# Optimization experiments

Measured on AMD Instinct MI355X. Metric: run time of the kernel, lower is better.

Reference implementation:

```python
import jax, jax.numpy as jnp
import numpy as np

HIDDEN = 2048
N_HEADS = 32
N_KV_HEADS = 4
HEAD_DIM = 128
EPS = 1e-6
ROPE_THETA = 1000000.0
B, S = 1, 2048


def setup_inputs() -> dict:
    key = jax.random.key(0)
    ks = jax.random.split(key, 7)
    scale = 0.02
    return {
        "hidden_states": jax.random.normal(ks[0], (B, S, HIDDEN), jnp.float32),
        "wq": jax.random.normal(ks[1], (HIDDEN, N_HEADS * HEAD_DIM), jnp.float32) * scale,
        "wk": jax.random.normal(ks[2], (HIDDEN, N_KV_HEADS * HEAD_DIM), jnp.float32) * scale,
        "wv": jax.random.normal(ks[3], (HIDDEN, N_KV_HEADS * HEAD_DIM), jnp.float32) * scale,
        "wo": jax.random.normal(ks[4], (N_HEADS * HEAD_DIM, HIDDEN), jnp.float32) * scale,
        "q_norm_w": jnp.ones((HEAD_DIM,), jnp.float32),
        "k_norm_w": jnp.ones((HEAD_DIM,), jnp.float32),
    }


def _rmsnorm(x, w, eps=EPS):
    # RMSNorm over last (head_dim) axis, as in Qwen3MoeRMSNorm applied per-head
    var = jnp.mean(jnp.square(x), axis=-1, keepdims=True)
    return x * jax.lax.rsqrt(var + eps) * w


def _rope_cos_sin(seq_len, dtype):
    inv_freq = 1.0 / (ROPE_THETA ** (jnp.arange(0, HEAD_DIM, 2, dtype=jnp.float32) / HEAD_DIM))
    pos = jnp.arange(seq_len, dtype=jnp.float32)
    freqs = pos[:, None] * inv_freq[None, :]          # [S, dh/2]
    emb = jnp.concatenate([freqs, freqs], axis=-1)    # [S, dh]
    return jnp.cos(emb).astype(dtype), jnp.sin(emb).astype(dtype)


def _rotate_half(x):
    h = x.shape[-1] // 2
    return jnp.concatenate([-x[..., h:], x[..., :h]], axis=-1)


def reference(hidden_states, wq, wk, wv, wo, q_norm_w, k_norm_w):
    b, s, _ = hidden_states.shape
    # QKV projections (bias-free)
    q = (hidden_states @ wq).reshape(b, s, N_HEADS, HEAD_DIM)
    k = (hidden_states @ wk).reshape(b, s, N_KV_HEADS, HEAD_DIM)
    v = (hidden_states @ wv).reshape(b, s, N_KV_HEADS, HEAD_DIM)
    # per-head RMSNorm on Q and K
    q = _rmsnorm(q, q_norm_w)
    k = _rmsnorm(k, k_norm_w)
    # RoPE (prefill, start_pos = 0)
    cos, sin = _rope_cos_sin(s, q.dtype)              # [S, dh]
    cos = cos[None, :, None, :]
    sin = sin[None, :, None, :]
    q = q * cos + _rotate_half(q) * sin
    k = k * cos + _rotate_half(k) * sin
    # GQA: repeat KV heads to match Q heads
    groups = N_HEADS // N_KV_HEADS
    k = jnp.repeat(k, groups, axis=2)                 # [B,S,nH,dh]
    v = jnp.repeat(v, groups, axis=2)
    # causal SDPA
    scaling = HEAD_DIM ** -0.5
    scores = jnp.einsum("bqhd,bkhd->bhqk", q, k) * scaling
    causal = jnp.tril(jnp.ones((s, s), dtype=bool))
    scores = jnp.where(causal[None, None], scores, jnp.finfo(scores.dtype).min)
    probs = jax.nn.softmax(scores, axis=-1)
    attn = jnp.einsum("bhqk,bkhd->bqhd", probs, v)    # [B,S,nH,dh]
    attn = attn.reshape(b, s, N_HEADS * HEAD_DIM)
    return attn @ wo
```

## Files before the change

kernel.cpp:

```cpp
#include <hip/hip_runtime.h>
#include <stdint.h>

typedef unsigned short u16;
typedef __bf16 bf16x8 __attribute__((ext_vector_type(8)));
typedef float f32x4 __attribute__((ext_vector_type(4)));

#define SEQ 2048
#define QKV_N 5120
#define QN 4096

#if __has_builtin(__builtin_amdgcn_exp2f)
#define EXP2F __builtin_amdgcn_exp2f
#else
#define EXP2F exp2f
#endif

#define QSC (0.08838834764831845f * 1.4426950408889634f)
#define MLOG2E 17.312340490667560f

__device__ __forceinline__ u16 f2bf(float f) {
  union { float f; unsigned u; } v; v.f = f;
  unsigned r = v.u + 0x7fffu + ((v.u >> 16) & 1u);
  return (u16)(r >> 16);
}
__device__ __forceinline__ u16 f2bf_fast(float f) {
  union { float f; unsigned u; } v; v.f = f;
  return (u16)((v.u + 0x8000u) >> 16);
}

__device__ __forceinline__ void gl2lds16(const void* g, void* l) {
  __builtin_amdgcn_global_load_lds((const __attribute__((address_space(1))) void*)g,
                                   (__attribute__((address_space(3))) void*)l, 16, 0, 0);
}

__global__ __launch_bounds__(256) void k_convert(const float* __restrict__ src, u16* __restrict__ dst) {
  int i = (blockIdx.x * 256 + threadIdx.x) * 4;
  float4 v = *(const float4*)(src + i);
  ushort4 o;
  o.x = f2bf(v.x); o.y = f2bf(v.y); o.z = f2bf(v.z); o.w = f2bf(v.w);
  *(ushort4*)(dst + i) = o;
}

__global__ __launch_bounds__(256) void k_transpose(const float* __restrict__ src, u16* __restrict__ dst,
                                                   int R, int C) {
  __shared__ float t[32][33];
  int c0 = blockIdx.x * 32, r0 = blockIdx.y * 32;
  int j = threadIdx.x & 31, i0 = threadIdx.x >> 5;
#pragma unroll
  for (int p = 0; p < 4; ++p) {
    int r = i0 + p * 8;
    t[r][j] = src[(size_t)(r0 + r) * C + c0 + j];
  }
  __syncthreads();
#pragma unroll
  for (int p = 0; p < 4; ++p) {
    int r = i0 + p * 8;
    dst[(size_t)(c0 + r) * R + r0 + j] = f2bf(t[j][r]);
  }
}

__global__ __launch_bounds__(256) void k_gemm_bt(const u16* __restrict__ A, const u16* __restrict__ BT,
                                                 float* __restrict__ C, int M, int N, int K) {
  __shared__ u16 As[128 * 64];
  __shared__ u16 Bs[128 * 64];
  const int tid = threadIdx.x;
  const int w = tid >> 6, lane = tid & 63, quad = lane >> 4, l15 = lane & 15;
  const int m0 = blockIdx.y * 128, n0 = blockIdx.x * 128;
  const int mw = (w & 1) * 64, nw = (w >> 1) * 64;

  f32x4 acc[4][4];
#pragma unroll
  for (int i = 0; i < 4; ++i)
#pragma unroll
    for (int j = 0; j < 4; ++j) acc[i][j] = {0.f, 0.f, 0.f, 0.f};

  const int nk = K >> 6;
  for (int kt = 0; kt < nk; ++kt) {
    const int k0 = kt << 6;
    __syncthreads();
#pragma unroll
    for (int p = 0; p < 4; ++p) {
      int ci = (w * 4 + p) * 64 + lane;
      int row = ci >> 3, pc = ci & 7, gc = pc ^ (row & 7);
      gl2lds16(A + (size_t)(m0 + row) * K + k0 + gc * 8, As + (w * 4 + p) * 512);
      gl2lds16(BT + (size_t)(n0 + row) * K + k0 + gc * 8, Bs + (w * 4 + p) * 512);
    }
    __syncthreads();
#pragma unroll
    for (int kk = 0; kk < 2; ++kk) {
      bf16x8 a[4], b[4];
#pragma unroll
      for (int mt = 0; mt < 4; ++mt) {
        int row = mw + mt * 16 + l15;
        int col = ((kk * 4 + quad) ^ (row & 7)) * 8;
        a[mt] = *(const bf16x8*)(As + row * 64 + col);
      }
#pragma unroll
      for (int nt = 0; nt < 4; ++nt) {
        int row = nw + nt * 16 + l15;
        int col = ((kk * 4 + quad) ^ (row & 7)) * 8;
        b[nt] = *(const bf16x8*)(Bs + row * 64 + col);
      }
#pragma unroll
      for (int mt = 0; mt < 4; ++mt)
#pragma unroll
        for (int nt = 0; nt < 4; ++nt)
          acc[mt][nt] = __builtin_amdgcn_mfma_f32_16x16x32_bf16(a[mt], b[nt], acc[mt][nt], 0, 0, 0);
    }
  }
#pragma unroll
  for (int mt = 0; mt < 4; ++mt)
#pragma unroll
    for (int nt = 0; nt < 4; ++nt)
#pragma unroll
      for (int r = 0; r < 4; ++r) {
        int row = m0 + mw + mt * 16 + quad * 4 + r;
        int col = n0 + nw + nt * 16 + l15;
        C[(size_t)row * N + col] = acc[mt][nt][r];
      }
}

__global__ __launch_bounds__(256) void k_gemm_bt64(const u16* __restrict__ A, const u16* __restrict__ BT,
                                                   float* __restrict__ C, int M, int N, int K) {
  __shared__ u16 As[64 * 64];
  __shared__ u16 Bs[128 * 64];
  const int tid = threadIdx.x;
  const int w = tid >> 6, lane = tid & 63, quad = lane >> 4, l15 = lane & 15;
  const int m0 = blockIdx.y * 64, n0 = blockIdx.x * 128;
  const int nw = w * 32;

  f32x4 acc[4][2];
#pragma unroll
  for (int i = 0; i < 4; ++i)
#pragma unroll
    for (int j = 0; j < 2; ++j) acc[i][j] = {0.f, 0.f, 0.f, 0.f};

  const int nk = K >> 6;
  for (int kt = 0; kt < nk; ++kt) {
    const int k0 = kt << 6;
    __syncthreads();
#pragma unroll
    for (int p = 0; p < 2; ++p) {
      int ci = p * 256 + tid;
      int row = ci >> 3, gc = (ci & 7) ^ (row & 7);
      gl2lds16(A + (size_t)(m0 + row) * K + k0 + gc * 8, As + (p * 256 + w * 64) * 8);
    }
#pragma unroll
    for (int p = 0; p < 4; ++p) {
      int ci = p * 256 + tid;
      int row = ci >> 3, gc = (ci & 7) ^ (row & 7);
      gl2lds16(BT + (size_t)(n0 + row) * K + k0 + gc * 8, Bs + (p * 256 + w * 64) * 8);
    }
    __syncthreads();
#pragma unroll
    for (int kk = 0; kk < 2; ++kk) {
      bf16x8 a[4], b[2];
#pragma unroll
      for (int mt = 0; mt < 4; ++mt) {
        int row = mt * 16 + l15;
        a[mt] = *(const bf16x8*)(As + row * 64 + (((kk * 4 + quad) ^ (row & 7)) * 8));
      }
#pragma unroll
      for (int nt = 0; nt < 2; ++nt) {
        int row = nw + nt * 16 + l15;
        b[nt] = *(const bf16x8*)(Bs + row * 64 + (((kk * 4 + quad) ^ (row & 7)) * 8));
      }
#pragma unroll
      for (int mt = 0; mt < 4; ++mt)
#pragma unroll
        for (int nt = 0; nt < 2; ++nt)
          acc[mt][nt] = __builtin_amdgcn_mfma_f32_16x16x32_bf16(a[mt], b[nt], acc[mt][nt], 0, 0, 0);
    }
  }
#pragma unroll
  for (int mt = 0; mt < 4; ++mt)
#pragma unroll
    for (int nt = 0; nt < 2; ++nt)
#pragma unroll
      for (int r = 0; r < 4; ++r) {
        int row = m0 + mt * 16 + quad * 4 + r;
        int col = n0 + nw + nt * 16 + l15;
        C[(size_t)row * N + col] = acc[mt][nt][r];
      }
}

__global__ __launch_bounds__(256) void k_postproc(const float* __restrict__ QKV,
                                                  const float* __restrict__ qw, const float* __restrict__ kw,
                                                  u16* __restrict__ qb, u16* __restrict__ kb) {
  int s = blockIdx.x;
  int w = threadIdx.x >> 6, lane = threadIdx.x & 63;
  const float* row = QKV + (size_t)s * QKV_N;
  float inv_freq = EXP2F(-(float)lane * (19.931568569324174f / 64.0f));
  float fr = (float)s * inv_freq;
  float sn, cs;
  __sincosf(fr, &sn, &cs);
  float qw0 = qw[lane], qw1 = qw[lane + 64];
  float kw0 = kw[lane], kw1 = kw[lane + 64];
  for (int item = w; item < 36; item += 4) {
    bool isq = item < 32;
    int h = isq ? item : item - 32;
    int base = isq ? h * 128 : 4096 + h * 128;
    float x0 = row[base + lane], x1 = row[base + 64 + lane];
    float ss = x0 * x0 + x1 * x1;
#pragma unroll
    for (int off = 1; off < 64; off <<= 1) ss += __shfl_xor(ss, off);
    float rr = rsqrtf(ss * (1.0f / 128.0f) + 1e-6f);
    float n0 = x0 * rr * (isq ? qw0 : kw0), n1 = x1 * rr * (isq ? qw1 : kw1);
    float y0 = n0 * cs - n1 * sn;
    float y1 = n1 * cs + n0 * sn;
    if (isq) {
      size_t o = (size_t)s * QN + h * 128 + lane;
      qb[o] = f2bf(y0 * QSC);
      qb[o + 64] = f2bf(y1 * QSC);
    } else {
      size_t o = ((size_t)h * SEQ + s) * 128 + lane;
      kb[o] = f2bf(y0);
      kb[o + 64] = f2bf(y1);
    }
  }
}

__global__ __launch_bounds__(256) void k_vtrans(const float* __restrict__ QKV, u16* __restrict__ vt) {
  __shared__ float t[32][33];
  int s0 = blockIdx.x * 32, d0 = blockIdx.y * 32, h = blockIdx.z;
  int j = threadIdx.x & 31, i0 = threadIdx.x >> 5;
#pragma unroll
  for (int p = 0; p < 4; ++p) {
    int r = i0 + p * 8;
    t[r][j] = QKV[(size_t)(s0 + r) * QKV_N + 4608 + h * 128 + d0 + j];
  }
  __syncthreads();
#pragma unroll
  for (int p = 0; p < 4; ++p) {
    int r = i0 + p * 8;
    vt[((size_t)h * 128 + d0 + r) * SEQ + s0 + j] = f2bf(t[j][r]);
  }
}

__global__ __launch_bounds__(256, 2) void k_flash(const u16* __restrict__ qb_, const u16* __restrict__ kb,
                                                  const u16* __restrict__ vt, u16* __restrict__ attn) {
  __shared__ u16 Ks[64 * 128];
  __shared__ u16 Vts[128 * 64];
  __shared__ u16 Ps[4][2048];
  const int bx = blockIdx.x;
  const int slot = bx & 255, phase = bx >> 8;
  const int head = slot & 31;
  const int qblk = phase ? (slot >> 5) : 15 - (slot >> 5);
  const int kvh = head >> 3;
  const int q0 = qblk * 128;
  const int tid = threadIdx.x, w = tid >> 6, lane = tid & 63, quad = lane >> 4, l15 = lane & 15;
  const int rowlo0 = q0 + w * 32, rowlo1 = rowlo0 + 16;

  bf16x8 qf[2][4];
#pragma unroll
  for (int mt = 0; mt < 2; ++mt) {
    const u16* qrow = qb_ + (size_t)(rowlo0 + mt * 16 + l15) * QN + head * 128;
#pragma unroll
    for (int ks = 0; ks < 4; ++ks) qf[mt][ks] = *(const bf16x8*)(qrow + ks * 32 + quad * 8);
  }
  f32x4 o[2][8];
#pragma unroll
  for (int mt = 0; mt < 2; ++mt)
#pragma unroll
    for (int i = 0; i < 8; ++i) o[mt][i] = {0.f, 0.f, 0.f, 0.f};
  float lr[2][4] = {{0.f, 0.f, 0.f, 0.f}, {0.f, 0.f, 0.f, 0.f}};

  const u16* kbase = kb + (size_t)kvh * SEQ * 128;
  const u16* vbase = vt + (size_t)kvh * 128 * SEQ;
  u16* pw = Ps[w];

  const int nT = 2 * qblk + 2;
  for (int ti = 0; ti < nT; ++ti) {
    const int t0 = ti * 64;
    __syncthreads();
#pragma unroll
    for (int p = 0; p < 4; ++p) {
      int ci = (w * 4 + p) * 64 + lane;
      {
        int row = ci >> 4, pc = ci & 15, gc = pc ^ (row & 15);
        gl2lds16(kbase + (size_t)(t0 + row) * 128 + gc * 8, Ks + (w * 4 + p) * 512);
      }
      {
        int d = ci >> 3, pc = ci & 7, gc = pc ^ (d & 7);
        gl2lds16(vbase + (size_t)d * SEQ + t0 + gc * 8, Vts + (w * 4 + p) * 512);
      }
    }
    __syncthreads();

    const bool a0 = t0 < rowlo0 + 16;
    const bool a1 = t0 < rowlo1 + 16;
    if (a1) {
      f32x4 sa[2][4];
#pragma unroll
      for (int mt = 0; mt < 2; ++mt)
#pragma unroll
        for (int nt = 0; nt < 4; ++nt) sa[mt][nt] = {0.f, 0.f, 0.f, 0.f};
#pragma unroll
      for (int nt = 0; nt < 4; ++nt) {
        int row = nt * 16 + l15;
#pragma unroll
        for (int ks = 0; ks < 4; ++ks) {
          bf16x8 kf = *(const bf16x8*)(Ks + row * 128 + (((ks * 4 + quad) ^ (row & 15)) * 8));
          if (a0) sa[0][nt] = __builtin_amdgcn_mfma_f32_16x16x32_bf16(qf[0][ks], kf, sa[0][nt], 0, 0, 0);
          sa[1][nt] = __builtin_amdgcn_mfma_f32_16x16x32_bf16(qf[1][ks], kf, sa[1][nt], 0, 0, 0);
        }
      }
#pragma unroll
      for (int mt = 0; mt < 2; ++mt) {
        if (mt == 0 && !a0) continue;
        const int rl = rowlo0 + mt * 16;
        const bool domask = (t0 + 63 > rl);
        u16* pm = pw + mt * 1024;
#pragma unroll
        for (int nt = 0; nt < 4; ++nt)
#pragma unroll
          for (int r = 0; r < 4; ++r) {
            float p = EXP2F(sa[mt][nt][r] - MLOG2E);
            if (domask) {
              int tcol = t0 + nt * 16 + l15;
              int qrow = rl + quad * 4 + r;
              p = (tcol > qrow) ? 0.f : p;
            }
            sa[mt][nt][r] = p;
            pm[(quad * 4 + r) * 64 + ((nt ^ quad) << 4) + l15] = f2bf_fast(p);
          }
#pragma unroll
        for (int r = 0; r < 4; ++r)
          lr[mt][r] += sa[mt][0][r] + sa[mt][1][r] + sa[mt][2][r] + sa[mt][3][r];
      }
      asm volatile("s_waitcnt lgkmcnt(0)" ::: "memory");
#pragma unroll
      for (int ks2 = 0; ks2 < 2; ++ks2) {
        int col = (ks2 * 32 + quad * 8) ^ ((l15 >> 2) << 4);
        bf16x8 pa0, pa1;
        if (a0) pa0 = *(const bf16x8*)(pw + l15 * 64 + col);
        pa1 = *(const bf16x8*)(pw + 1024 + l15 * 64 + col);
#pragma unroll
        for (int nt2 = 0; nt2 < 8; ++nt2) {
          int d = nt2 * 16 + l15;
          bf16x8 vf = *(const bf16x8*)(Vts + d * 64 + (((ks2 * 4 + quad) ^ (d & 7)) * 8));
          if (a0) o[0][nt2] = __builtin_amdgcn_mfma_f32_16x16x32_bf16(pa0, vf, o[0][nt2], 0, 0, 0);
          o[1][nt2] = __builtin_amdgcn_mfma_f32_16x16x32_bf16(pa1, vf, o[1][nt2], 0, 0, 0);
        }
      }
    }
  }
#pragma unroll
  for (int mt = 0; mt < 2; ++mt) {
    float inv[4];
#pragma unroll
    for (int r = 0; r < 4; ++r) {
      float s = lr[mt][r];
      s += __shfl_xor(s, 1);
      s += __shfl_xor(s, 2);
      s += __shfl_xor(s, 4);
      s += __shfl_xor(s, 8);
      inv[r] = 1.0f / s;
    }
#pragma unroll
    for (int nt2 = 0; nt2 < 8; ++nt2)
#pragma unroll
      for (int r = 0; r < 4; ++r) {
        size_t idx = (size_t)(rowlo0 + mt * 16 + quad * 4 + r) * QN + head * 128 + nt2 * 16 + l15;
        attn[idx] = f2bf_fast(o[mt][nt2][r] * inv[r]);
      }
  }
}

extern "C" void kernel_launch(void* const* d_in, const int* in_sizes, int n_in,
                              void* d_out, int out_size, void* d_ws, size_t ws_size,
                              hipStream_t stream) {
  const float* hidden = (const float*)d_in[0];
  const float* wq = (const float*)d_in[1];
  const float* wk = (const float*)d_in[2];
  const float* wv = (const float*)d_in[3];
  const float* wo = (const float*)d_in[4];
  const float* qnw = (const float*)d_in[5];
  const float* knw = (const float*)d_in[6];
  float* out = (float*)d_out;

  char* ws = (char*)d_ws;
  u16* hid_bf = (u16*)(ws);
  u16* WT = (u16*)(ws + 8388608);
  u16* woT = (u16*)(ws + 29360128);
  float* QKV = (float*)(ws + 46137344);
  u16* q_bf = (u16*)(ws + 88080384);
  u16* k_bf = (u16*)(ws + 104857600);
  u16* vt = (u16*)(ws + 106954752);
  u16* attn = (u16*)(ws + 109051904);

  k_convert<<<4096, 256, 0, stream>>>(hidden, hid_bf);
  k_transpose<<<dim3(128, 64), 256, 0, stream>>>(wq, WT, 2048, 4096);
  k_transpose<<<dim3(16, 64), 256, 0, stream>>>(wk, WT + (size_t)4096 * 2048, 2048, 512);
  k_transpose<<<dim3(16, 64), 256, 0, stream>>>(wv, WT + (size_t)4608 * 2048, 2048, 512);
  k_transpose<<<dim3(64, 128), 256, 0, stream>>>(wo, woT, 4096, 2048);
  k_gemm_bt<<<dim3(40, 16), 256, 0, stream>>>(hid_bf, WT, QKV, 2048, 5120, 2048);
  k_postproc<<<2048, 256, 0, stream>>>(QKV, qnw, knw, q_bf, k_bf);
  k_vtrans<<<dim3(64, 4, 4), 256, 0, stream>>>(QKV, vt);
  k_flash<<<512, 256, 0, stream>>>(q_bf, k_bf, vt, attn);
  k_gemm_bt64<<<dim3(16, 32), 256, 0, stream>>>(attn, woT, out, 2048, 2048, 4096);
}
```

Measured before the change: 362.1 us.

## Retile QKV GEMM to 160-wide tiles with bf16 output and split-K output projection

The QKV projection now uses 128x160 tiles, giving a 32x16 grid of 512 blocks instead of 640, and stores bf16 rather than fp32. This halves the QKV intermediate traffic read by the postprocess and V-transpose kernels. The output projection switches from 64-row tiles to 128x128 tiles with split-K over two halves, accumulating with atomicAdd into an output zeroed by a memset. In exchange it adds an extra memset, atomic write traffic, and bf16 rounding of the QKV values before RMSNorm.

Result: faster. 340.9 us (-5.9%).

```diff
diff --git a/kernel.cpp b/kernel.cpp
--- a/kernel.cpp
+++ b/kernel.cpp
@@ -26,6 +26,10 @@
 __device__ __forceinline__ u16 f2bf_fast(float f) {
   union { float f; unsigned u; } v; v.f = f;
   return (u16)((v.u + 0x8000u) >> 16);
+}
+__device__ __forceinline__ float bf2f(u16 b) {
+  union { unsigned u; float f; } v; v.u = ((unsigned)b) << 16;
+  return v.f;
 }
 
 __device__ __forceinline__ void gl2lds16(const void* g, void* l) {
@@ -59,7 +63,71 @@
   }
 }
 
-__global__ __launch_bounds__(256) void k_gemm_bt(const u16* __restrict__ A, const u16* __restrict__ BT,
+__global__ __launch_bounds__(256) void k_gemm160(const u16* __restrict__ A, const u16* __restrict__ BT,
+                                                 u16* __restrict__ C, int M, int N, int K) {
+  __shared__ u16 As[128 * 64];
+  __shared__ u16 Bs[160 * 64];
+  const int tid = threadIdx.x;
+  const int w = tid >> 6, lane = tid & 63, quad = lane >> 4, l15 = lane & 15;
+  const int m0 = blockIdx.y * 128, n0 = blockIdx.x * 160;
+  const int mw = (w & 1) * 64, nw = (w >> 1) * 80;
+
+  f32x4 acc[4][5];
+#pragma unroll
+  for (int i = 0; i < 4; ++i)
+#pragma unroll
+    for (int j = 0; j < 5; ++j) acc[i][j] = {0.f, 0.f, 0.f, 0.f};
+
+  const int nk = K >> 6;
+  for (int kt = 0; kt < nk; ++kt) {
+    const int k0 = kt << 6;
+    __syncthreads();
+#pragma unroll
+    for (int p = 0; p < 4; ++p) {
+      int ci = (w * 4 + p) * 64 + lane;
+      int row = ci >> 3, gc = (ci & 7) ^ (row & 7);
+      gl2lds16(A + (size_t)(m0 + row) * K + k0 + gc * 8, As + (w * 4 + p) * 512);
+    }
+#pragma unroll
+    for (int p = 0; p < 5; ++p) {
+      int ci = (w * 5 + p) * 64 + lane;
+      int row = ci >> 3, gc = (ci & 7) ^ (row & 7);
+      gl2lds16(BT + (size_t)(n0 + row) * K + k0 + gc * 8, Bs + (w * 5 + p) * 512);
+    }
+    __syncthreads();
+#pragma unroll
+    for (int kk = 0; kk < 2; ++kk) {
+      bf16x8 a[4], b[5];
+#pragma unroll
+      for (int mt = 0; mt < 4; ++mt) {
+        int row = mw + mt * 16 + l15;
+        a[mt] = *(const bf16x8*)(As + row * 64 + (((kk * 4 + quad) ^ (row & 7)) * 8));
+      }
+#pragma unroll
+      for (int nt = 0; nt < 5; ++nt) {
+        int row = nw + nt * 16 + l15;
+        b[nt] = *(const bf16x8*)(Bs + row * 64 + (((kk * 4 + quad) ^ (row & 7)) * 8));
+      }
+#pragma unroll
+      for (int mt = 0; mt < 4; ++mt)
+#pragma unroll
+        for (int nt = 0; nt < 5; ++nt)
+          acc[mt][nt] = __builtin_amdgcn_mfma_f32_16x16x32_bf16(a[mt], b[nt], acc[mt][nt], 0, 0, 0);
+    }
+  }
+#pragma unroll
+  for (int mt = 0; mt < 4; ++mt)
+#pragma unroll
+    for (int nt = 0; nt < 5; ++nt)
+#pragma unroll
+      for (int r = 0; r < 4; ++r) {
+        int row = m0 + mw + mt * 16 + quad * 4 + r;
+        int col = n0 + nw + nt * 16 + l15;
+        C[(size_t)row * N + col] = f2bf(acc[mt][nt][r]);
+      }
+}
+
+__global__ __launch_bounds__(256) void k_gemm_sk(const u16* __restrict__ A, const u16* __restrict__ BT,
                                                  float* __restrict__ C, int M, int N, int K) {
   __shared__ u16 As[128 * 64];
   __shared__ u16 Bs[128 * 64];
@@ -67,6 +135,8 @@
   const int w = tid >> 6, lane = tid & 63, quad = lane >> 4, l15 = lane & 15;
   const int m0 = blockIdx.y * 128, n0 = blockIdx.x * 128;
   const int mw = (w & 1) * 64, nw = (w >> 1) * 64;
+  const int khalf = K >> 1;
+  const int kbase = blockIdx.z * khalf;
 
   f32x4 acc[4][4];
 #pragma unroll
@@ -74,14 +144,14 @@
 #pragma unroll
     for (int j = 0; j < 4; ++j) acc[i][j] = {0.f, 0.f, 0.f, 0.f};
 
-  const int nk = K >> 6;
+  const int nk = khalf >> 6;
   for (int kt = 0; kt < nk; ++kt) {
-    const int k0 = kt << 6;
+    const int k0 = kbase + (kt << 6);
     __syncthreads();
 #pragma unroll
     for (int p = 0; p < 4; ++p) {
       int ci = (w * 4 + p) * 64 + lane;
-      int row = ci >> 3, pc = ci & 7, gc = pc ^ (row & 7);
+      int row = ci >> 3, gc = (ci & 7) ^ (row & 7);
       gl2lds16(A + (size_t)(m0 + row) * K + k0 + gc * 8, As + (w * 4 + p) * 512);
       gl2lds16(BT + (size_t)(n0 + row) * K + k0 + gc * 8, Bs + (w * 4 + p) * 512);
     }
@@ -92,14 +162,12 @@
 #pragma unroll
       for (int mt = 0; mt < 4; ++mt) {
         int row = mw + mt * 16 + l15;
-        int col = ((kk * 4 + quad) ^ (row & 7)) * 8;
-        a[mt] = *(const bf16x8*)(As + row * 64 + col);
+        a[mt] = *(const bf16x8*)(As + row * 64 + (((kk * 4 + quad) ^ (row & 7)) * 8));
       }
 #pragma unroll
       for (int nt = 0; nt < 4; ++nt) {
         int row = nw + nt * 16 + l15;
-        int col = ((kk * 4 + quad) ^ (row & 7)) * 8;
-        b[nt] = *(const bf16x8*)(Bs + row * 64 + col);
+        b[nt] = *(const bf16x8*)(Bs + row * 64 + (((kk * 4 + quad) ^ (row & 7)) * 8));
       }
 #pragma unroll
       for (int mt = 0; mt < 4; ++mt)
@@ -116,80 +184,16 @@
       for (int r = 0; r < 4; ++r) {
         int row = m0 + mw + mt * 16 + quad * 4 + r;
         int col = n0 + nw + nt * 16 + l15;
-        C[(size_t)row * N + col] = acc[mt][nt][r];
-      }
-}
-
-__global__ __launch_bounds__(256) void k_gemm_bt64(const u16* __restrict__ A, const u16* __restrict__ BT,
-                                                   float* __restrict__ C, int M, int N, int K) {
-  __shared__ u16 As[64 * 64];
-  __shared__ u16 Bs[128 * 64];
-  const int tid = threadIdx.x;
-  const int w = tid >> 6, lane = tid & 63, quad = lane >> 4, l15 = lane & 15;
-  const int m0 = blockIdx.y * 64, n0 = blockIdx.x * 128;
-  const int nw = w * 32;
-
-  f32x4 acc[4][2];
-#pragma unroll
-  for (int i = 0; i < 4; ++i)
-#pragma unroll
-    for (int j = 0; j < 2; ++j) acc[i][j] = {0.f, 0.f, 0.f, 0.f};
-
-  const int nk = K >> 6;
-  for (int kt = 0; kt < nk; ++kt) {
-    const int k0 = kt << 6;
-    __syncthreads();
-#pragma unroll
-    for (int p = 0; p < 2; ++p) {
-      int ci = p * 256 + tid;
-      int row = ci >> 3, gc = (ci & 7) ^ (row & 7);
-      gl2lds16(A + (size_t)(m0 + row) * K + k0 + gc * 8, As + (p * 256 + w * 64) * 8);
-    }
-#pragma unroll
-    for (int p = 0; p < 4; ++p) {
-      int ci = p * 256 + tid;
-      int row = ci >> 3, gc = (ci & 7) ^ (row & 7);
-      gl2lds16(BT + (size_t)(n0 + row) * K + k0 + gc * 8, Bs + (p * 256 + w * 64) * 8);
-    }
-    __syncthreads();
-#pragma unroll
-    for (int kk = 0; kk < 2; ++kk) {
-      bf16x8 a[4], b[2];
-#pragma unroll
-      for (int mt = 0; mt < 4; ++mt) {
-        int row = mt * 16 + l15;
-        a[mt] = *(const bf16x8*)(As + row * 64 + (((kk * 4 + quad) ^ (row & 7)) * 8));
-      }
-#pragma unroll
-      for (int nt = 0; nt < 2; ++nt) {
-        int row = nw + nt * 16 + l15;
-        b[nt] = *(const bf16x8*)(Bs + row * 64 + (((kk * 4 + quad) ^ (row & 7)) * 8));
-      }
-#pragma unroll
-      for (int mt = 0; mt < 4; ++mt)
-#pragma unroll
-        for (int nt = 0; nt < 2; ++nt)
-          acc[mt][nt] = __builtin_amdgcn_mfma_f32_16x16x32_bf16(a[mt], b[nt], acc[mt][nt], 0, 0, 0);
-    }
-  }
-#pragma unroll
-  for (int mt = 0; mt < 4; ++mt)
-#pragma unroll
-    for (int nt = 0; nt < 2; ++nt)
-#pragma unroll
-      for (int r = 0; r < 4; ++r) {
-        int row = m0 + mt * 16 + quad * 4 + r;
-        int col = n0 + nw + nt * 16 + l15;
-        C[(size_t)row * N + col] = acc[mt][nt][r];
-      }
-}
-
-__global__ __launch_bounds__(256) void k_postproc(const float* __restrict__ QKV,
+        atomicAdd(&C[(size_t)row * N + col], acc[mt][nt][r]);
+      }
+}
+
+__global__ __launch_bounds__(256) void k_postproc(const u16* __restrict__ QKV,
                                                   const float* __restrict__ qw, const float* __restrict__ kw,
                                                   u16* __restrict__ qb, u16* __restrict__ kb) {
   int s = blockIdx.x;
   int w = threadIdx.x >> 6, lane = threadIdx.x & 63;
-  const float* row = QKV + (size_t)s * QKV_N;
+  const u16* row = QKV + (size_t)s * QKV_N;
   float inv_freq = EXP2F(-(float)lane * (19.931568569324174f / 64.0f));
   float fr = (float)s * inv_freq;
   float sn, cs;
@@ -200,7 +204,7 @@
     bool isq = item < 32;
     int h = isq ? item : item - 32;
     int base = isq ? h * 128 : 4096 + h * 128;
-    float x0 = row[base + lane], x1 = row[base + 64 + lane];
+    float x0 = bf2f(row[base + lane]), x1 = bf2f(row[base + 64 + lane]);
     float ss = x0 * x0 + x1 * x1;
 #pragma unroll
     for (int off = 1; off < 64; off <<= 1) ss += __shfl_xor(ss, off);
@@ -220,8 +224,8 @@
   }
 }
 
-__global__ __launch_bounds__(256) void k_vtrans(const float* __restrict__ QKV, u16* __restrict__ vt) {
-  __shared__ float t[32][33];
+__global__ __launch_bounds__(256) void k_vtrans(const u16* __restrict__ QKV, u16* __restrict__ vt) {
+  __shared__ u16 t[32][34];
   int s0 = blockIdx.x * 32, d0 = blockIdx.y * 32, h = blockIdx.z;
   int j = threadIdx.x & 31, i0 = threadIdx.x >> 5;
 #pragma unroll
@@ -233,7 +237,7 @@
 #pragma unroll
   for (int p = 0; p < 4; ++p) {
     int r = i0 + p * 8;
-    vt[((size_t)h * 128 + d0 + r) * SEQ + s0 + j] = f2bf(t[j][r]);
+    vt[((size_t)h * 128 + d0 + r) * SEQ + s0 + j] = t[j][r];
   }
 }
 
@@ -383,20 +387,21 @@
   u16* hid_bf = (u16*)(ws);
   u16* WT = (u16*)(ws + 8388608);
   u16* woT = (u16*)(ws + 29360128);
-  float* QKV = (float*)(ws + 46137344);
+  u16* QKV = (u16*)(ws + 46137344);
   u16* q_bf = (u16*)(ws + 88080384);
   u16* k_bf = (u16*)(ws + 104857600);
   u16* vt = (u16*)(ws + 106954752);
   u16* attn = (u16*)(ws + 109051904);
 
+  hipMemsetAsync(d_out, 0, (size_t)2048 * 2048 * 4, stream);
   k_convert<<<4096, 256, 0, stream>>>(hidden, hid_bf);
   k_transpose<<<dim3(128, 64), 256, 0, stream>>>(wq, WT, 2048, 4096);
   k_transpose<<<dim3(16, 64), 256, 0, stream>>>(wk, WT + (size_t)4096 * 2048, 2048, 512);
   k_transpose<<<dim3(16, 64), 256, 0, stream>>>(wv, WT + (size_t)4608 * 2048, 2048, 512);
   k_transpose<<<dim3(64, 128), 256, 0, stream>>>(wo, woT, 4096, 2048);
-  k_gemm_bt<<<dim3(40, 16), 256, 0, stream>>>(hid_bf, WT, QKV, 2048, 5120, 2048);
+  k_gemm160<<<dim3(32, 16), 256, 0, stream>>>(hid_bf, WT, QKV, 2048, 5120, 2048);
   k_postproc<<<2048, 256, 0, stream>>>(QKV, qnw, knw, q_bf, k_bf);
   k_vtrans<<<dim3(64, 4, 4), 256, 0, stream>>>(QKV, vt);
   k_flash<<<512, 256, 0, stream>>>(q_bf, k_bf, vt, attn);
-  k_gemm_bt64<<<dim3(16, 32), 256, 0, stream>>>(attn, woT, out, 2048, 2048, 4096);
-}
+  k_gemm_sk<<<dim3(16, 16, 2), 256, 0, stream>>>(attn, woT, out, 2048, 2048, 4096);
+}
```
